# Kernel tuning notes

Measured on AMD Instinct MI355X. Metric: run time of the kernel, lower is better.

The kernel has to match this reference:

```python
import jax, jax.numpy as jnp
import numpy as np

# 1x1 Conv2d == channel contraction
def _conv(x, w):
    return jnp.einsum('bctn,oc->botn', x, w)

# BatchNorm2d in eval mode; p rows = (gamma, beta, running_mean, running_var)
def _bn(x, p, eps=1e-5):
    g, b, m, v = p
    s = g * jax.lax.rsqrt(v + eps)
    return x * s[None, :, None, None] + (b - m * s)[None, :, None, None]


def _forward(x, pos_2d, w_pos, b_pos, w_expand, bn_expand, w1, bn1, w2, bn2,
             w_ag, bn_ag, w_ag_s, b_ag_s, w_att, bn_att, w_att_s, b_att_s, W):
    B, T, J, Cp, N = x.shape
    C = J * Cp
    # rearrange 'b t j c n -> b (j c) t n'
    f = x.transpose(0, 2, 3, 1, 4).reshape(B, C, T, N)
    # pairwise expansion: h[b,:,t,i,j] = concat(f[b,:,t,i], f[b,:,t,j])  -> (B,2C,T,N*N)
    x1 = jnp.broadcast_to(f[:, :, :, :, None], (B, C, T, N, N))
    x2 = jnp.broadcast_to(f[:, :, :, None, :], (B, C, T, N, N))
    h = jnp.concatenate([x1, x2], axis=1).reshape(B, 2 * C, T, N * N)
    # relative 2D position embedding (first 2 coord channels)
    p = pos_2d[:, :, :, :2, :].transpose(0, 2, 3, 1, 4).reshape(B, 2 * J, T, N)
    rel = (p[:, :, :, :, None] - p[:, :, :, None, :]).reshape(B, 2 * J, T, N * N)
    pos_emb = _conv(rel, w_pos) + b_pos[None, :, None, None]
    # VAL trunk (dropout = identity in eval)
    h = jax.nn.relu(_bn(_conv(h, w_expand), bn_expand)) + pos_emb
    res = h
    h = jax.nn.relu(_bn(_conv(h, w1), bn1))
    h = jax.nn.relu(_bn(_conv(h, w2), bn2))
    h = res + h
    ag = _conv(jax.nn.relu(_bn(_conv(h, w_ag), bn_ag)), w_ag_s) + b_ag_s[None, :, None, None]
    ag = ag.reshape(B, -1, T, N, N)          # (B,Co,T,N,N)
    att = _conv(jax.nn.relu(_bn(_conv(h, w_att), bn_att)), w_att_s) + b_att_s[None, :, None, None]
    att = att.reshape(B, 1, T, N, N)
    # self / transfer terms, broadcast over receiver axis i
    f_self = jnp.einsum('bctn,cd->bdtn', f, W[0])[:, :, :, None, :]  # (B,Co,T,1,N)
    f_tran = jnp.einsum('bctn,cd->bdtn', f, W[1])[:, :, :, None, :] * ag
    E = jnp.eye(N, dtype=f.dtype)[None, None, None]                  # (1,1,1,N,N)
    f_conv = E * f_self + (1.0 - E) * f_tran
    att = jax.nn.softmax(att, axis=-1)
    f_fuse = jnp.sum(f_conv * att, axis=-1) + f                      # (B,Co,T,N)
    return f_fuse.reshape(B, J, Cp, T, N).transpose(0, 3, 1, 2, 4)   # (B,T,J,Cp,N)


def setup_inputs() -> dict:
    key = jax.random.key(0)
    ks = iter(jax.random.split(key, 64))
    B, T, J, Cp, N = 8, 128, 17, 32, 4
    C = J * Cp            # 544
    Cin = 2 * C           # 1088 (VAL in_channels)
    Co = C                # 544 (out_channels)

    def w(shape, s=0.03):
        return jax.random.normal(next(ks), shape, jnp.float32) * s

    def bn(c):
        return jnp.stack([
            1.0 + 0.1 * jax.random.normal(next(ks), (c,), jnp.float32),
            0.1 * jax.random.normal(next(ks), (c,), jnp.float32),
            0.1 * jax.random.normal(next(ks), (c,), jnp.float32),
            0.5 + jax.random.uniform(next(ks), (c,), jnp.float32),
        ])

    return dict(
        x=jax.random.normal(next(ks), (B, T, J, Cp, N), jnp.float32),
        pos_2d=jax.random.normal(next(ks), (B, T, J, 2, N), jnp.float32),
        w_pos=w((Cin, 2 * J)), b_pos=w((Cin,)),
        w_expand=w((Cin, Cin)), bn_expand=bn(Cin),
        w1=w((Cin, Cin)), bn1=bn(Cin),
        w2=w((Cin, Cin)), bn2=bn(Cin),
        w_ag=w((Cin, Cin)), bn_ag=bn(Cin),
        w_ag_s=w((Co, Cin)), b_ag_s=w((Co,)),
        w_att=w((Cin, Cin)), bn_att=bn(Cin),
        w_att_s=w((1, Cin)), b_att_s=w((1,)),
        W=w((2, Co, Co), 0.05),
    )


def reference(x, pos_2d, w_pos, b_pos, w_expand, bn_expand, w1, bn1, w2, bn2,
              w_ag, bn_ag, w_ag_s, b_ag_s, w_att, bn_att, w_att_s, b_att_s, W):
    return _forward(x, pos_2d, w_pos, b_pos, w_expand, bn_expand, w1, bn1, w2, bn2,
                    w_ag, bn_ag, w_ag_s, b_ag_s, w_att, bn_att, w_att_s, b_att_s, W)
```

## Files before the change

### kernel.cpp

```cpp
#include <hip/hip_runtime.h>

typedef unsigned short u16;
typedef unsigned int   u32;
typedef __attribute__((ext_vector_type(4))) float f32x4;
typedef __attribute__((ext_vector_type(8))) short short8;

#define DI static __device__ __forceinline__

DI u16 f2bf(float x){ union{float f;u32 u;}v; v.f=x; u32 r=v.u + 0x7fffu + ((v.u>>16)&1u); return (u16)(r>>16); }
DI float bf2f(u16 h){ union{u32 u;float f;}v; v.u=((u32)h)<<16; return v.f; }

DI void gl_lds16(const u16* g, u16* l){
  __builtin_amdgcn_global_load_lds((const __attribute__((address_space(1))) void*)g,
                                   (__attribute__((address_space(3))) void*)l, 16, 0, 0);
}


__global__ void k_bnprep(const float* __restrict__ bnE, const float* __restrict__ bn1,
                         const float* __restrict__ bn2, const float* __restrict__ bnA,
                         const float* __restrict__ bnT, float* __restrict__ out){
  int i = blockIdx.x*256 + threadIdx.x;
  if(i >= 5*1088) return;
  int w = i/1088, c = i - w*1088;
  const float* b = (w==0)?bnE:(w==1)?bn1:(w==2)?bn2:(w==3)?bnA:bnT;
  float g=b[c], be=b[1088+c], mu=b[2176+c], va=b[3264+c];
  float s = g / sqrtf(va + 1e-5f);
  out[w*2176 + c] = s;
  out[w*2176 + 1088 + c] = be - mu*s;
}

__global__ void k_zero(float* p, int n){ int i = blockIdx.x*256+threadIdx.x; if(i<n) p[i]=0.f; }

__global__ void k_pack_f(const float* __restrict__ x, float* __restrict__ fmat,
                         u16* __restrict__ fhi, u16* __restrict__ flo){
  int bt = blockIdx.x;
  const float* xr = x + (size_t)bt*2176;
  for(int t=threadIdx.x; t<2176; t+=256){
    int c = t>>2, n = t&3;
    float v = xr[t];
    size_t o = (size_t)(bt*4+n)*544 + c;
    fmat[o] = v;
    u16 h = f2bf(v); fhi[o]=h; flo[o]=f2bf(v - bf2f(h));
  }
}

__global__ void k_pack_w(const float* __restrict__ src, int off1, int off2, int O1,
                         int rs, int cs, int O, int K,
                         u16* __restrict__ dhi, u16* __restrict__ dlo){
  int o = blockIdx.y;
  int k = blockIdx.x*256 + threadIdx.x;
  if(k >= K) return;
  float v = 0.f;
  if(o < O){
    size_t idx = (o<O1) ? (size_t)off1 + (size_t)o*rs + (size_t)k*cs
                        : (size_t)off2 + (size_t)(o-O1)*rs + (size_t)k*cs;
    v = src[idx];
  }
  size_t d = (size_t)o*K + k;
  u16 h=f2bf(v); dhi[d]=h; dlo[d]=f2bf(v - bf2f(h));
}

__global__ void k_q(const float* __restrict__ pos, const float* __restrict__ w_pos,
                    float* __restrict__ q){
  int m = blockIdx.x; int bt = m>>2, n = m&3;
  __shared__ float pr[34];
  if(threadIdx.x<34){ int j = threadIdx.x>>1, d = threadIdx.x&1;
    pr[threadIdx.x] = pos[(size_t)bt*136 + j*8 + d*4 + n]; }
  __syncthreads();
  for(int o=threadIdx.x;o<1088;o+=256){
    const float* wr = w_pos + (size_t)o*34;
    float s = 0.f;
    #pragma unroll
    for(int k=0;k<34;k++) s += pr[k]*wr[k];
    q[(size_t)m*1088 + o] = s;
  }
}

__global__ void k_expand(const float* __restrict__ uv, const float* __restrict__ q,
                         const float* __restrict__ bn, const float* __restrict__ b_pos,
                         u16* __restrict__ hh, u16* __restrict__ hl){
  __shared__ float su[4][1088], sv[4][1088], sq[4][1088];
  int bt = blockIdx.x;
  for(int t=threadIdx.x; t<4*1088; t+=256){
    int r = t/1088, o = t - r*1088;
    su[r][o] = uv[(size_t)(bt*4+r)*2176 + o];
    sv[r][o] = uv[(size_t)(bt*4+r)*2176 + 1088 + o];
    sq[r][o] = q[(size_t)(bt*4+r)*1088 + o];
  }
  __syncthreads();
  for(int t=threadIdx.x; t<16*1088; t+=256){
    int ij = t/1088, o = t - ij*1088; int i = ij>>2, j = ij&3;
    float xv = bn[o]*(su[i][o]+sv[j][o]) + bn[1088+o];
    xv = fmaxf(xv,0.f) + sq[i][o]-sq[j][o]+b_pos[o];
    size_t idx = (size_t)(bt*16+ij)*1088 + o;
    u16 h=f2bf(xv); hh[idx]=h; hl[idx]=f2bf(xv-bf2f(h));
  }
}

template<int EPI>
__global__ __launch_bounds__(256,2)
void k_gemm(const u16* __restrict__ Ahi, const u16* __restrict__ Alo,
            const u16* __restrict__ Bhi, const u16* __restrict__ Blo,
            int K, int Nout, int ldo,
            float* __restrict__ out_f, u16* __restrict__ out_hi, u16* __restrict__ out_lo,
            const float* __restrict__ sv, const float* __restrict__ tv,
            const u16* __restrict__ res_hi, const u16* __restrict__ res_lo,
            const float* __restrict__ bias,
            const float* __restrict__ wred, float* __restrict__ red_out)
{
  __shared__ u16 Ah[2][4096], Al[2][4096], Bh[2][4096], Bl[2][4096];
  __shared__ float red[128];
  const int tid = threadIdx.x, lane = tid&63, wave = tid>>6;
  const int wm = wave>>1, wn = wave&1;
  const int m0 = blockIdx.x*128, n0 = blockIdx.y*128;
  if(EPI==4 && tid<128) red[tid]=0.f;

  auto stage = [&](int buf, int kt){
    const int k0 = kt*32;
    #pragma unroll
    for(int c=0;c<2;c++){
      int s   = (wave*2+c)*64 + lane;
      int row = s>>2;
      int kg  = (s&3) ^ ((row>>1)&3);
      size_t ga = (size_t)(m0+row)*K + k0 + kg*8;
      size_t gb = (size_t)(n0+row)*K + k0 + kg*8;
      int lo = (wave*2+c)*512;
      gl_lds16(Ahi+ga, &Ah[buf][lo]);
      gl_lds16(Alo+ga, &Al[buf][lo]);
      gl_lds16(Bhi+gb, &Bh[buf][lo]);
      gl_lds16(Blo+gb, &Bl[buf][lo]);
    }
  };

  f32x4 acc[4][4];
  #pragma unroll
  for(int i=0;i<4;i++)
    #pragma unroll
    for(int j=0;j<4;j++){ acc[i][j][0]=0.f; acc[i][j][1]=0.f; acc[i][j][2]=0.f; acc[i][j][3]=0.f; }

  const int NT = K>>5;
  stage(0,0);
  __syncthreads();
  int buf = 0;
  const int swz = ((lane>>4) ^ (((lane&15)>>1)&3))<<3;
  const int iA = ((wm*64 + (lane&15))<<5) + swz;
  const int iB = ((wn*64 + (lane&15))<<5) + swz;

  for(int kt=0; kt<NT; ++kt){
    if(kt+1<NT) stage(buf^1, kt+1);
    short8 ah[4],al[4],bh[4],bl[4];
    #pragma unroll
    for(int i=0;i<4;i++){
      ah[i] = *(const short8*)&Ah[buf][iA + i*512];
      al[i] = *(const short8*)&Al[buf][iA + i*512];
      bh[i] = *(const short8*)&Bh[buf][iB + i*512];
      bl[i] = *(const short8*)&Bl[buf][iB + i*512];
    }
    #pragma unroll
    for(int mi=0;mi<4;mi++)
      #pragma unroll
      for(int ni=0;ni<4;ni++){
        acc[mi][ni] = __builtin_amdgcn_mfma_f32_16x16x32_bf16(ah[mi],bh[ni],acc[mi][ni],0,0,0);
        acc[mi][ni] = __builtin_amdgcn_mfma_f32_16x16x32_bf16(al[mi],bh[ni],acc[mi][ni],0,0,0);
        acc[mi][ni] = __builtin_amdgcn_mfma_f32_16x16x32_bf16(ah[mi],bl[ni],acc[mi][ni],0,0,0);
      }
    __syncthreads();
    buf ^= 1;
  }

  const int r0 = m0 + wm*64 + ((lane>>4)<<2);
  const int c0 = n0 + wn*64 + (lane&15);

  if constexpr (EPI==0){
    #pragma unroll
    for(int mi=0;mi<4;mi++)
      #pragma unroll
      for(int ni=0;ni<4;ni++){
        int col = c0 + ni*16;
        if(col < Nout){
          #pragma unroll
          for(int r=0;r<4;r++)
            out_f[(size_t)(r0+mi*16+r)*ldo + col] = acc[mi][ni][r];
        }
      }
  } else if constexpr (EPI==1 || EPI==2){
    #pragma unroll
    for(int mi=0;mi<4;mi++)
      #pragma unroll
      for(int ni=0;ni<4;ni++){
        int col = c0 + ni*16;
        if(col < Nout){
          float sc = sv[col], tc = tv[col];
          #pragma unroll
          for(int r=0;r<4;r++){
            float y = fmaxf(acc[mi][ni][r]*sc + tc, 0.f);
            size_t idx = (size_t)(r0+mi*16+r)*ldo + col;
            if(EPI==2) y += bf2f(res_hi[idx]) + bf2f(res_lo[idx]);
            u16 h = f2bf(y); out_hi[idx]=h; out_lo[idx]=f2bf(y - bf2f(h));
          }
        }
      }
  } else if constexpr (EPI==3){
    #pragma unroll
    for(int mi=0;mi<4;mi++)
      #pragma unroll
      for(int ni=0;ni<4;ni++){
        int col = c0 + ni*16;
        if(col < Nout){
          float bc = bias[col];
          #pragma unroll
          for(int r=0;r<4;r++)
            out_f[(size_t)(r0+mi*16+r)*ldo + col] = acc[mi][ni][r] + bc;
        }
      }
  } else {
    float rs4[4][4];
    #pragma unroll
    for(int mi=0;mi<4;mi++)
      #pragma unroll
      for(int r=0;r<4;r++) rs4[mi][r]=0.f;
    #pragma unroll
    for(int mi=0;mi<4;mi++)
      #pragma unroll
      for(int ni=0;ni<4;ni++){
        int col = c0 + ni*16;
        if(col < Nout){
          float sc = sv[col], tc = tv[col], wc = wred[col];
          #pragma unroll
          for(int r=0;r<4;r++)
            rs4[mi][r] += fmaxf(acc[mi][ni][r]*sc + tc, 0.f)*wc;
        }
      }
    #pragma unroll
    for(int off=1; off<16; off<<=1)
      #pragma unroll
      for(int mi=0;mi<4;mi++)
        #pragma unroll
        for(int r=0;r<4;r++)
          rs4[mi][r] += __shfl_xor(rs4[mi][r], off, 64);
    if((lane&15)==0){
      #pragma unroll
      for(int mi=0;mi<4;mi++)
        #pragma unroll
        for(int r=0;r<4;r++)
          atomicAdd(&red[wm*64 + mi*16 + ((lane>>4)<<2) + r], rs4[mi][r]);
    }
    __syncthreads();
    if(tid<128) atomicAdd(&red_out[m0+tid], red[tid]);
  }
}

__global__ void k_fuse(const float* __restrict__ logits, const float* __restrict__ ag,
                       const float* __restrict__ fsft, const float* __restrict__ fmat,
                       float* __restrict__ out){
  int bt = blockIdx.x;
  float a[4][4];
  #pragma unroll
  for(int i=0;i<4;i++){
    float l0=logits[bt*16+i*4+0], l1=logits[bt*16+i*4+1],
          l2=logits[bt*16+i*4+2], l3=logits[bt*16+i*4+3];
    float mx = fmaxf(fmaxf(l0,l1),fmaxf(l2,l3));
    float e0=__expf(l0-mx), e1=__expf(l1-mx), e2=__expf(l2-mx), e3=__expf(l3-mx);
    float inv = 1.f/(e0+e1+e2+e3);
    a[i][0]=e0*inv; a[i][1]=e1*inv; a[i][2]=e2*inv; a[i][3]=e3*inv;
  }
  for(int d=threadIdx.x; d<544; d+=256){
    float fsv[4], ftv[4], fv[4];
    #pragma unroll
    for(int j=0;j<4;j++){
      fsv[j] = fsft[(size_t)(bt*4+j)*1088 + d];
      ftv[j] = fsft[(size_t)(bt*4+j)*1088 + 544 + d];
      fv[j]  = fmat[(size_t)(bt*4+j)*544 + d];
    }
    float o4[4];
    #pragma unroll
    for(int i=0;i<4;i++){
      float s = fv[i];
      #pragma unroll
      for(int j=0;j<4;j++){
        float fc = (j==i) ? fsv[j] : ftv[j]*ag[(size_t)(bt*16+i*4+j)*544 + d];
        s += a[i][j]*fc;
      }
      o4[i]=s;
    }
    *(float4*)(out + ((size_t)bt*544 + d)*4) = make_float4(o4[0],o4[1],o4[2],o4[3]);
  }
}

extern "C" void kernel_launch(void* const* d_in, const int* in_sizes, int n_in,
                              void* d_out, int out_size, void* d_ws, size_t ws_size,
                              hipStream_t stream){
  (void)in_sizes; (void)n_in; (void)out_size; (void)ws_size;
  const float* x      = (const float*)d_in[0];
  const float* pos2d  = (const float*)d_in[1];
  const float* w_pos  = (const float*)d_in[2];
  const float* b_pos  = (const float*)d_in[3];
  const float* w_exp  = (const float*)d_in[4];
  const float* bnE    = (const float*)d_in[5];
  const float* w1     = (const float*)d_in[6];
  const float* bn1    = (const float*)d_in[7];
  const float* w2     = (const float*)d_in[8];
  const float* bn2    = (const float*)d_in[9];
  const float* w_ag   = (const float*)d_in[10];
  const float* bnA    = (const float*)d_in[11];
  const float* w_ag_s = (const float*)d_in[12];
  const float* b_ag_s = (const float*)d_in[13];
  const float* w_att  = (const float*)d_in[14];
  const float* bnT    = (const float*)d_in[15];
  const float* w_att_s= (const float*)d_in[16];
  const float* Wm     = (const float*)d_in[18];
  float* out = (float*)d_out;

  char* ws = (char*)d_ws;
  size_t off = 0;
  auto alloc = [&](size_t b)->char*{ char* p = ws+off; off += (b+255)&~(size_t)255; return p; };

  float* fmat  = (float*)alloc(8912896);
  u16*   fhi   = (u16*)  alloc(4456448);
  u16*   flo   = (u16*)  alloc(4456448);
  float* bnbuf = (float*)alloc(43520);
  u16*   wuv   = (u16*)  alloc(5013504);
  u16*   w1p   = (u16*)  alloc(5013504);
  u16*   w2p   = (u16*)  alloc(5013504);
  u16*   wagp  = (u16*)  alloc(5013504);
  u16*   watp  = (u16*)  alloc(5013504);
  u16*   wagsp = (u16*)  alloc(2785280);
  u16*   wWp   = (u16*)  alloc(2506752);
  float* logits= (float*)alloc(65536);
  char*  X0    = alloc(71303168);
  char*  X1    = alloc(71303168);
  char*  X2    = alloc(71303168);

  u16* h0h=(u16*)X0;            u16* h0l=(u16*)(X0+35651584);
  u16* a1h=(u16*)X0;            u16* a1l=(u16*)(X0+35651584);
  float* qb =(float*)X1;
  u16* r1h=(u16*)X1;            u16* r1l=(u16*)(X1+35651584);
  float* agb =(float*)X1;       float* fsft=(float*)(X1+35651584);
  float* uvb =(float*)X2;
  u16* h2h=(u16*)X2;            u16* h2l=(u16*)(X2+35651584);

  k_bnprep<<<22,256,0,stream>>>(bnE,bn1,bn2,bnA,bnT,bnbuf);
  k_zero  <<<64,256,0,stream>>>(logits,16384);
  k_pack_f<<<1024,256,0,stream>>>(x, fmat, fhi, flo);
  k_pack_w<<<dim3(3,2304),256,0,stream>>>(w_exp, 0,544,1088, 1088,1, 2176,544, wuv, wuv+2304*544);
  k_pack_w<<<dim3(5,1152),256,0,stream>>>(w1,   0,0,1088, 1088,1, 1088,1088, w1p, w1p+1152*1088);
  k_pack_w<<<dim3(5,1152),256,0,stream>>>(w2,   0,0,1088, 1088,1, 1088,1088, w2p, w2p+1152*1088);
  k_pack_w<<<dim3(5,1152),256,0,stream>>>(w_ag, 0,0,1088, 1088,1, 1088,1088, wagp, wagp+1152*1088);
  k_pack_w<<<dim3(5,1152),256,0,stream>>>(w_att,0,0,1088, 1088,1, 1088,1088, watp, watp+1152*1088);
  k_pack_w<<<dim3(5, 640),256,0,stream>>>(w_ag_s,0,0, 544, 1088,1,  544,1088, wagsp, wagsp+640*1088);
  k_pack_w<<<dim3(3,1152),256,0,stream>>>(Wm, 0,544*544,544, 1,544, 1088,544, wWp, wWp+1152*544);
  k_q<<<4096,256,0,stream>>>(pos2d, w_pos, qb);

  k_gemm<0><<<dim3(32,18),256,0,stream>>>(fhi,flo, wuv,wuv+2304*544, 544, 2176, 2176,
      uvb, nullptr,nullptr, nullptr,nullptr, nullptr,nullptr, nullptr, nullptr,nullptr);
  k_expand<<<1024,256,0,stream>>>(uvb, qb, bnbuf, b_pos, h0h, h0l);
  k_gemm<1><<<dim3(128,9),256,0,stream>>>(h0h,h0l, w1p,w1p+1152*1088, 1088, 1088, 1088,
      nullptr, r1h,r1l, bnbuf+2176, bnbuf+2176+1088, nullptr,nullptr, nullptr, nullptr,nullptr);
  k_gemm<2><<<dim3(128,9),256,0,stream>>>(r1h,r1l, w2p,w2p+1152*1088, 1088, 1088, 1088,
      nullptr, h2h,h2l, bnbuf+2*2176, bnbuf+2*2176+1088, h0h,h0l, nullptr, nullptr,nullptr);
  k_gemm<1><<<dim3(128,9),256,0,stream>>>(h2h,h2l, wagp,wagp+1152*1088, 1088, 1088, 1088,
      nullptr, a1h,a1l, bnbuf+3*2176, bnbuf+3*2176+1088, nullptr,nullptr, nullptr, nullptr,nullptr);
  k_gemm<3><<<dim3(128,5),256,0,stream>>>(a1h,a1l, wagsp,wagsp+640*1088, 1088, 544, 544,
      agb, nullptr,nullptr, nullptr,nullptr, nullptr,nullptr, b_ag_s, nullptr,nullptr);
  k_gemm<4><<<dim3(128,9),256,0,stream>>>(h2h,h2l, watp,watp+1152*1088, 1088, 1088, 1088,
      nullptr, nullptr,nullptr, bnbuf+4*2176, bnbuf+4*2176+1088, nullptr,nullptr, nullptr,
      w_att_s, logits);
  k_gemm<0><<<dim3(32,9),256,0,stream>>>(fhi,flo, wWp,wWp+1152*544, 544, 1088, 1088,
      fsft, nullptr,nullptr, nullptr,nullptr, nullptr,nullptr, nullptr, nullptr,nullptr);
  k_fuse<<<1024,256,0,stream>>>(logits, agb, fsft, fmat, out);
}
```

Baseline: 1.004 ms.

## Deepen GEMM prefetch pipeline with explicit waitcnt barriers and XCD-aware block remap

Restructures the k_gemm main loop so two K-tiles are in flight. Each iteration loads LDS fragments to registers, barriers, then issues the global->LDS stage for tile kt+2 into the just-freed buffer before running the MFMAs at raised priority, waiting with vmcnt(8) instead of a full sync. The MFMA loops are reordered so each hi/lo product pass runs across all 16 accumulators, and block indices are remapped so consecutive tiles land on the same XCD for L2 reuse. The clamped redundant stage at the tail adds some wasted loads, and the remap assumes the grid size is divisible by 8.

```diff
diff --git a/kernel.cpp b/kernel.cpp
--- a/kernel.cpp
+++ b/kernel.cpp
@@ -112,7 +112,13 @@
   __shared__ float red[128];
   const int tid = threadIdx.x, lane = tid&63, wave = tid>>6;
   const int wm = wave>>1, wn = wave&1;
-  const int m0 = blockIdx.x*128, n0 = blockIdx.y*128;
+
+  const int gx = gridDim.x, gy = gridDim.y;
+  const int flat = blockIdx.y*gx + blockIdx.x;
+  const int chunk = (gx*gy) >> 3;
+  const int p = (flat & 7)*chunk + (flat >> 3);
+  const int bx = p/gy, by = p - bx*gy;
+  const int m0 = bx*128, n0 = by*128;
   if(EPI==4 && tid<128) red[tid]=0.f;
 
   auto stage = [&](int buf, int kt){
@@ -140,14 +146,17 @@
 
   const int NT = K>>5;
   stage(0,0);
-  __syncthreads();
-  int buf = 0;
+  stage(1,1);
+  asm volatile("s_waitcnt vmcnt(8)" ::: "memory");
+  __builtin_amdgcn_sched_barrier(0);
+  __builtin_amdgcn_s_barrier();
+
   const int swz = ((lane>>4) ^ (((lane&15)>>1)&3))<<3;
   const int iA = ((wm*64 + (lane&15))<<5) + swz;
   const int iB = ((wn*64 + (lane&15))<<5) + swz;
 
   for(int kt=0; kt<NT; ++kt){
-    if(kt+1<NT) stage(buf^1, kt+1);
+    const int buf = kt&1;
     short8 ah[4],al[4],bh[4],bl[4];
     #pragma unroll
     for(int i=0;i<4;i++){
@@ -156,16 +165,31 @@
       bh[i] = *(const short8*)&Bh[buf][iB + i*512];
       bl[i] = *(const short8*)&Bl[buf][iB + i*512];
     }
-    #pragma unroll
-    for(int mi=0;mi<4;mi++)
-      #pragma unroll
-      for(int ni=0;ni<4;ni++){
+    asm volatile("s_waitcnt lgkmcnt(0)" ::: "memory");
+    __builtin_amdgcn_sched_barrier(0);
+    __builtin_amdgcn_s_barrier();
+    int kt2 = kt+2; if(kt2 > NT-1) kt2 = NT-1;
+    stage(buf, kt2);
+    __builtin_amdgcn_s_setprio(1);
+    #pragma unroll
+    for(int mi=0;mi<4;mi++)
+      #pragma unroll
+      for(int ni=0;ni<4;ni++)
         acc[mi][ni] = __builtin_amdgcn_mfma_f32_16x16x32_bf16(ah[mi],bh[ni],acc[mi][ni],0,0,0);
+    #pragma unroll
+    for(int mi=0;mi<4;mi++)
+      #pragma unroll
+      for(int ni=0;ni<4;ni++)
         acc[mi][ni] = __builtin_amdgcn_mfma_f32_16x16x32_bf16(al[mi],bh[ni],acc[mi][ni],0,0,0);
+    #pragma unroll
+    for(int mi=0;mi<4;mi++)
+      #pragma unroll
+      for(int ni=0;ni<4;ni++)
         acc[mi][ni] = __builtin_amdgcn_mfma_f32_16x16x32_bf16(ah[mi],bl[ni],acc[mi][ni],0,0,0);
-      }
-    __syncthreads();
-    buf ^= 1;
+    __builtin_amdgcn_s_setprio(0);
+    asm volatile("s_waitcnt vmcnt(8)" ::: "memory");
+    __builtin_amdgcn_sched_barrier(0);
+    __builtin_amdgcn_s_barrier();
   }
 
   const int r0 = m0 + wm*64 + ((lane>>4)<<2);
```

Result: faster. 935.7 us (-6.8%).
